# Optimization experiments

Measured on AMD Instinct MI355X. Metric: run time of the kernel, lower is better.

Reference implementation:

```python
import jax, jax.numpy as jnp
import numpy as np

GROUPS = 8
HEADS = 4
EPS = 1e-5


def setup_inputs() -> dict:
    key = jax.random.key(0)
    ks = jax.random.split(key, 3)
    b, c, h, w = 4, 256, 64, 64
    x = jax.random.normal(ks[0], (b, c, h, w), dtype=jnp.float32)
    gn_gamma = jnp.ones((c,), jnp.float32)
    gn_beta = jnp.zeros((c,), jnp.float32)
    w_qkv = jax.random.normal(ks[1], (3 * c, c), dtype=jnp.float32) * (c ** -0.5)
    w_proj = jax.random.normal(ks[2], (c, c), dtype=jnp.float32) * (c ** -0.5)
    b_proj = jnp.zeros((c,), jnp.float32)
    return {"x": x, "gn_gamma": gn_gamma, "gn_beta": gn_beta,
            "w_qkv": w_qkv, "w_proj": w_proj, "b_proj": b_proj}


def reference(x, gn_gamma, gn_beta, w_qkv, w_proj, b_proj):
    b, c, h, w = x.shape
    residual = x
    # GroupNorm(8, c)
    xg = x.reshape(b, GROUPS, -1)
    mean = jnp.mean(xg, axis=-1, keepdims=True)
    var = jnp.var(xg, axis=-1, keepdims=True)
    xn = ((xg - mean) * jax.lax.rsqrt(var + EPS)).reshape(b, c, h, w)
    xn = xn * gn_gamma[:, None, None] + gn_beta[:, None, None]
    # QKV conv1x1 (no bias)
    qkv = jnp.einsum('oc,bchw->bohw', w_qkv, xn)  # [b,3c,h,w]
    q, k, v = jnp.split(qkv, 3, axis=1)
    n = h * w
    dh = c // HEADS
    q = q.reshape(b, HEADS, dh, n)
    k = k.reshape(b, HEADS, dh, n)
    v = v.reshape(b, HEADS, dh, n)
    scale = (c * HEADS) ** (-0.5)
    attn = jnp.einsum('bhci,bhcj->bhij', q, k) * scale  # [b,H,n,n]
    attn = jax.nn.softmax(attn, axis=-1)
    out = jnp.einsum('bhij,bhcj->bhci', attn, v).reshape(b, c, h, w)
    out = jnp.einsum('oc,bchw->bohw', w_proj, out) + b_proj[:, None, None]
    return out + residual
```

## Files before the change

kernel.cpp:

```cpp
#include <hip/hip_runtime.h>
#include <math.h>
#include <stdint.h>

#define B_ 4
#define C_ 256
#define HW_ 4096
#define G_ 8
#define H_ 4
#define DH_ 64
#define GRP_ELEMS (32 * HW_)
#define NCHUNK 16
#define CHUNK_ELEMS (GRP_ELEMS / NCHUNK)
#define EPS 1e-5f
#define NT_ (HW_ / 64)
#define QSCALE 0.04508422f

typedef __attribute__((ext_vector_type(8))) short short8;
typedef __attribute__((ext_vector_type(4))) float f32x4;
typedef __attribute__((ext_vector_type(4))) unsigned int u32x4;
typedef const __attribute__((address_space(1))) uint32_t* gas1_t;
typedef __attribute__((address_space(3))) uint32_t* las3_t;

__device__ __forceinline__ ushort f2bf(float x) {
    unsigned u = __builtin_bit_cast(unsigned, x);
    u += 0x7FFFu + ((u >> 16) & 1u);
    return (ushort)(u >> 16);
}
__device__ __forceinline__ uint32_t cvt_pk_bf16(float lo, float hi) {
    uint32_t r;
    asm("v_cvt_pk_bf16_f32 %0, %1, %2" : "=v"(r) : "v"(lo), "v"(hi));
    return r;
}

__global__ __launch_bounds__(256) void gn_part_wcvt(const float* __restrict__ x,
                                                    float* __restrict__ part,
                                                    const float* __restrict__ wq,
                                                    const float* __restrict__ wp,
                                                    ushort* __restrict__ wqb,
                                                    ushort* __restrict__ wpb) {
    int t = threadIdx.x;
    if (blockIdx.x >= 512) {
        int i = (blockIdx.x - 512) * 256 + t;
        if (i < 768 * 256) {
            float s = (i < 256 * 256) ? QSCALE : 1.0f;
            wqb[i] = f2bf(wq[i] * s);
        } else {
            wpb[i - 768 * 256] = f2bf(wp[i - 768 * 256]);
        }
        return;
    }
    int bg = blockIdx.x >> 4;
    int chunk = blockIdx.x & 15;
    const float4* p = (const float4*)(x + (size_t)bg * GRP_ELEMS + (size_t)chunk * CHUNK_ELEMS);
    float s = 0.f, ss = 0.f;
#pragma unroll
    for (int i = 0; i < 8; ++i) {
        float4 v = p[t + i * 256];
        s  += v.x + v.y + v.z + v.w;
        ss += v.x * v.x + v.y * v.y + v.z * v.z + v.w * v.w;
    }
#pragma unroll
    for (int off = 32; off; off >>= 1) {
        s  += __shfl_xor(s, off, 64);
        ss += __shfl_xor(ss, off, 64);
    }
    __shared__ float ls[8];
    int wave = t >> 6, lane = t & 63;
    if (lane == 0) { ls[wave * 2] = s; ls[wave * 2 + 1] = ss; }
    __syncthreads();
    if (t == 0) {
        float S = 0.f, SS = 0.f;
#pragma unroll
        for (int w = 0; w < 4; ++w) { S += ls[w * 2]; SS += ls[w * 2 + 1]; }
        part[(bg * 16 + chunk) * 2]     = S;
        part[(bg * 16 + chunk) * 2 + 1] = SS;
    }
}

#define TSTR 264
__global__ __launch_bounds__(256) void gn_qkv(const float* __restrict__ x,
                                              const float* __restrict__ gamma,
                                              const float* __restrict__ beta,
                                              const float* __restrict__ part,
                                              const ushort* __restrict__ wqb,
                                              ushort* __restrict__ qt,
                                              ushort* __restrict__ kt,
                                              ushort* __restrict__ vv) {
    __shared__ float2 affs[256];
    __shared__ __align__(16) ushort Ts[64 * TSTR];
    int n0 = blockIdx.x * 64;
    int b  = blockIdx.y;
    int t = threadIdx.x;

    {
        int c = t;
        int bg = b * G_ + (c >> 5);
        float S = 0.f, SS = 0.f;
#pragma unroll
        for (int i = 0; i < 16; ++i) {
            S  += part[(bg * 16 + i) * 2];
            SS += part[(bg * 16 + i) * 2 + 1];
        }
        float mean = S * (1.f / GRP_ELEMS);
        float var  = SS * (1.f / GRP_ELEMS) - mean * mean;
        float inv  = rsqrtf(var + EPS);
        float a = inv * gamma[c];
        affs[c] = make_float2(a, beta[c] - mean * a);
    }
    __syncthreads();

    {
        int n4 = t & 15, cr = t >> 4;
#pragma unroll
        for (int ct = 0; ct < 16; ++ct) {
            int c = cr + 16 * ct;
            float2 p = affs[c];
            float4 v = *(const float4*)(x + ((size_t)(b * C_ + c)) * HW_ + n0 + n4 * 4);
            ushort e[4];
            e[0] = f2bf(v.x * p.x + p.y); e[1] = f2bf(v.y * p.x + p.y);
            e[2] = f2bf(v.z * p.x + p.y); e[3] = f2bf(v.w * p.x + p.y);
#pragma unroll
            for (int k = 0; k < 4; ++k) {
                int n = n4 * 4 + k;
                Ts[n * TSTR + (((c >> 3) ^ ((n >> 2) & 7)) << 3) + (c & 7)] = e[k];
            }
        }
    }
    __syncthreads();

    int w = t >> 6, lane = t & 63, l16 = lane & 15, lg = lane >> 4;

    for (int z = 0; z < 3; ++z) {
        const ushort* wz = wqb + (size_t)(z * 256 + 32 * w + l16) * C_;
        f32x4 acc[2][2][4];
#pragma unroll
        for (int j = 0; j < 2; ++j)
#pragma unroll
            for (int os = 0; os < 2; ++os)
#pragma unroll
                for (int u = 0; u < 4; ++u)
#pragma unroll
                    for (int r = 0; r < 4; ++r) acc[j][os][u][r] = 0.f;

#pragma unroll 2
        for (int ks = 0; ks < 8; ++ks) {
            short8 a00 = *(const short8*)(wz + 32 * ks + 8 * lg);
            short8 a01 = *(const short8*)(wz + 16 * C_ + 32 * ks + 8 * lg);
            short8 a10 = *(const short8*)(wz + 128 * C_ + 32 * ks + 8 * lg);
            short8 a11 = *(const short8*)(wz + 144 * C_ + 32 * ks + 8 * lg);
#pragma unroll
            for (int u = 0; u < 4; ++u) {
                int n = 16 * u + l16;
                short8 bf = *(const short8*)&Ts[n * TSTR +
                               (((4 * ks + lg) ^ ((n >> 2) & 7)) << 3)];
                acc[0][0][u] = __builtin_amdgcn_mfma_f32_16x16x32_bf16(a00, bf, acc[0][0][u], 0, 0, 0);
                acc[0][1][u] = __builtin_amdgcn_mfma_f32_16x16x32_bf16(a01, bf, acc[0][1][u], 0, 0, 0);
                acc[1][0][u] = __builtin_amdgcn_mfma_f32_16x16x32_bf16(a10, bf, acc[1][0][u], 0, 0, 0);
                acc[1][1][u] = __builtin_amdgcn_mfma_f32_16x16x32_bf16(a11, bf, acc[1][1][u], 0, 0, 0);
            }
        }

#pragma unroll
        for (int j = 0; j < 2; ++j)
#pragma unroll
            for (int os = 0; os < 2; ++os) {
                int o_base = z * 256 + 128 * j + 32 * w + 16 * os;
                if (z < 2) {
                    int h = (o_base >> 6) & 3;
                    int od0 = (o_base & 63) + 4 * lg;
                    ushort* dstb = (z ? kt : qt) + ((size_t)((b << 2) | h) * HW_) * DH_;
#pragma unroll
                    for (int u = 0; u < 4; ++u) {
                        int n = n0 + 16 * u + l16;
                        uint2 pk;
                        pk.x = cvt_pk_bf16(acc[j][os][u][0], acc[j][os][u][1]);
                        pk.y = cvt_pk_bf16(acc[j][os][u][2], acc[j][os][u][3]);
                        *(uint2*)(dstb + (size_t)n * DH_ + od0) = pk;
                    }
                } else {
                    int row0 = o_base - 512 + 4 * lg;
#pragma unroll
                    for (int u = 0; u < 4; ++u) {
                        int n = n0 + 16 * u + l16;
#pragma unroll
                        for (int r = 0; r < 4; ++r)
                            vv[((size_t)(b * C_ + row0 + r)) * HW_ + n] = f2bf(acc[j][os][u][r]);
                    }
                }
            }
    }
}

__global__ __launch_bounds__(256) void flash_attn_mfma(const ushort* __restrict__ qt,
                                                       const ushort* __restrict__ kt,
                                                       const ushort* __restrict__ vv,
                                                       ushort* __restrict__ attT) {
    __shared__ __align__(16) ushort Kb[3][64 * 64];
    __shared__ __align__(16) ushort Vb[3][64 * 64];

    int bid = blockIdx.x;
    int wg = (bid & 7) * 64 + (bid >> 3);
    int bh = wg >> 5;
    int i0 = (wg & 31) * 128;
    int b = bh >> 2, h = bh & 3;
    int t = threadIdx.x;
    int w = t >> 6, lane = t & 63, l16 = lane & 15, lg = lane >> 4;
    const ushort* qtb = qt + (size_t)bh * HW_ * DH_;
    const ushort* ktb = kt + (size_t)bh * HW_ * DH_;
    const ushort* vb  = vv + ((size_t)(b * C_) + h * DH_) * HW_;

    short8 qf[2][2];
#pragma unroll
    for (int s = 0; s < 2; ++s)
#pragma unroll
        for (int ks = 0; ks < 2; ++ks)
            qf[s][ks] = *(const short8*)(qtb + (size_t)(i0 + 32 * w + 16 * s + l16) * DH_ + 32 * ks + 8 * lg);

    f32x4 O0[4], O1[4], lacc0, lacc1;
#pragma unroll
    for (int dt = 0; dt < 4; ++dt)
#pragma unroll
        for (int r = 0; r < 4; ++r) { O0[dt][r] = 0.f; O1[dt][r] = 0.f; }
#pragma unroll
    for (int r = 0; r < 4; ++r) { lacc0[r] = 0.f; lacc1[r] = 0.f; }
    const f32x4 Z4 = {0.f, 0.f, 0.f, 0.f};

    u32x4 ov; ov[0] = ov[1] = ov[2] = ov[3] = 0x3F803F80u;
    short8 onesf = __builtin_bit_cast(short8, ov);

    int r8 = lane >> 3, ch8 = lane & 7;
    size_t koff[2], voff[2];
#pragma unroll
    for (int half = 0; half < 2; ++half) {
        int L = 16 * w + half * 8 + r8;
        int gk = (L & 0x23) | ((L & 0x0C) << 1) | ((L & 0x10) >> 2);
        koff[half] = (size_t)gk * DH_ + ((ch8 ^ (L & 7)) << 3);
        voff[half] = (size_t)L * HW_ + ((ch8 ^ (L & 7)) << 3);
    }

    auto stageK = [&](int bi, int j0) {
#pragma unroll
        for (int half = 0; half < 2; ++half) {
            int rowb = 16 * w + half * 8;
            __builtin_amdgcn_global_load_lds((gas1_t)(ktb + (size_t)j0 * DH_ + koff[half]),
                (las3_t)&Kb[bi][rowb * 64], 16, 0, 0);
        }
    };
    auto stageV = [&](int bi, int j0) {
#pragma unroll
        for (int half = 0; half < 2; ++half) {
            int rowb = 16 * w + half * 8;
            __builtin_amdgcn_global_load_lds((gas1_t)(vb + (size_t)j0 + voff[half]),
                (las3_t)&Vb[bi][rowb * 64], 16, 0, 0);
        }
    };

    auto qk2 = [&](int bi, f32x4* S0, f32x4* S1) {
        __builtin_amdgcn_s_setprio(1);
#pragma unroll
        for (int jt = 0; jt < 4; ++jt) {
            short8 kf0 = *(const short8*)&Kb[bi][(16 * jt + l16) * 64 +
                                                ((lg ^ (l16 & 7)) << 3)];
            S0[jt] = __builtin_amdgcn_mfma_f32_16x16x32_bf16(kf0, qf[0][0], Z4, 0, 0, 0);
            S1[jt] = __builtin_amdgcn_mfma_f32_16x16x32_bf16(kf0, qf[1][0], Z4, 0, 0, 0);
            short8 kf1 = *(const short8*)&Kb[bi][(16 * jt + l16) * 64 +
                                                (((4 + lg) ^ (l16 & 7)) << 3)];
            S0[jt] = __builtin_amdgcn_mfma_f32_16x16x32_bf16(kf1, qf[0][1], S0[jt], 0, 0, 0);
            S1[jt] = __builtin_amdgcn_mfma_f32_16x16x32_bf16(kf1, qf[1][1], S1[jt], 0, 0, 0);
        }
        __builtin_amdgcn_s_setprio(0);
    };

    auto pv2 = [&](int bi, short8* pf0, short8* pf1) {
        __builtin_amdgcn_s_setprio(1);
#pragma unroll
        for (int dt = 0; dt < 4; ++dt) {
#pragma unroll
            for (int ks = 0; ks < 2; ++ks) {
                short8 vf = *(const short8*)&Vb[bi][(16 * dt + l16) * 64 +
                                                    (((4 * ks + lg) ^ (l16 & 7)) << 3)];
                O0[dt] = __builtin_amdgcn_mfma_f32_16x16x32_bf16(vf, pf0[ks], O0[dt], 0, 0, 0);
                O1[dt] = __builtin_amdgcn_mfma_f32_16x16x32_bf16(vf, pf1[ks], O1[dt], 0, 0, 0);
            }
        }
        lacc0 = __builtin_amdgcn_mfma_f32_16x16x32_bf16(onesf, pf0[0], lacc0, 0, 0, 0);
        lacc0 = __builtin_amdgcn_mfma_f32_16x16x32_bf16(onesf, pf0[1], lacc0, 0, 0, 0);
        lacc1 = __builtin_amdgcn_mfma_f32_16x16x32_bf16(onesf, pf1[0], lacc1, 0, 0, 0);
        lacc1 = __builtin_amdgcn_mfma_f32_16x16x32_bf16(onesf, pf1[1], lacc1, 0, 0, 0);
        __builtin_amdgcn_s_setprio(0);
    };

    auto softmax_pf = [&](f32x4* S, short8* pf) {
#pragma unroll
        for (int jt = 0; jt < 4; ++jt)
#pragma unroll
            for (int r = 0; r < 4; ++r)
                S[jt][r] = __builtin_amdgcn_exp2f(S[jt][r]);
#pragma unroll
        for (int ks = 0; ks < 2; ++ks) {
            u32x4 p;
            p[0] = cvt_pk_bf16(S[2 * ks][0],     S[2 * ks][1]);
            p[1] = cvt_pk_bf16(S[2 * ks][2],     S[2 * ks][3]);
            p[2] = cvt_pk_bf16(S[2 * ks + 1][0], S[2 * ks + 1][1]);
            p[3] = cvt_pk_bf16(S[2 * ks + 1][2], S[2 * ks + 1][3]);
            pf[ks] = __builtin_bit_cast(short8, p);
        }
    };

    f32x4 Sa0[4], Sa1[4], Sb0[4], Sb1[4];

    auto body = [&](int VW, int KR, int KW, int VR,
                    f32x4* SC0, f32x4* SC1, f32x4* SN0, f32x4* SN1,
                    int tt, int drain) {
        if (tt + 2 < NT_) stageV(VW, (tt + 2) * 64);
        qk2(KR, SN0, SN1);
        if (tt + 3 < NT_) stageK(KW, (tt + 3) * 64);
        short8 pf0[2], pf1[2];
        softmax_pf(SC0, pf0);
        softmax_pf(SC1, pf1);
        pv2(VR, pf0, pf1);
        if (drain == 4) asm volatile("s_waitcnt vmcnt(4)" ::: "memory");
        else            asm volatile("s_waitcnt vmcnt(0)" ::: "memory");
        __builtin_amdgcn_s_barrier();
    };

    stageK(0, 0); stageV(0, 0);
    stageK(1, 64); stageV(1, 64);
    stageK(2, 128);
    asm volatile("s_waitcnt vmcnt(0)" ::: "memory");
    __builtin_amdgcn_s_barrier();
    qk2(0, Sa0, Sa1);
    __builtin_amdgcn_s_barrier();

    for (int g = 0; g < 10; ++g) {
        int tb = 6 * g;
        body(2, 1, 0, 0, Sa0, Sa1, Sb0, Sb1, tb + 0, 4);
        body(0, 2, 1, 1, Sb0, Sb1, Sa0, Sa1, tb + 1, 4);
        body(1, 0, 2, 2, Sa0, Sa1, Sb0, Sb1, tb + 2, 4);
        body(2, 1, 0, 0, Sb0, Sb1, Sa0, Sa1, tb + 3, 4);
        body(0, 2, 1, 1, Sa0, Sa1, Sb0, Sb1, tb + 4, 4);
        body(1, 0, 2, 2, Sb0, Sb1, Sa0, Sa1, tb + 5, 4);
    }
    body(2, 1, 0, 0, Sa0, Sa1, Sb0, Sb1, 60, 4);
    body(0, 2, 1, 1, Sb0, Sb1, Sa0, Sa1, 61, 4);
    body(1, 0, 2, 2, Sa0, Sa1, Sb0, Sb1, 62, 0);
    {
        short8 pf0[2], pf1[2];
        softmax_pf(Sb0, pf0);
        softmax_pf(Sb1, pf1);
        pv2(0, pf0, pf1);
    }

    float inv0 = 1.f / lacc0[0], inv1 = 1.f / lacc1[0];
    ushort* ab0 = attT + ((size_t)b * HW_ + i0 + 32 * w + l16) * C_ + h * DH_;
    ushort* ab1 = ab0 + 16 * C_;
#pragma unroll
    for (int dt = 0; dt < 4; ++dt) {
        uint2 p0, p1;
        p0.x = cvt_pk_bf16(O0[dt][0] * inv0, O0[dt][1] * inv0);
        p0.y = cvt_pk_bf16(O0[dt][2] * inv0, O0[dt][3] * inv0);
        *(uint2*)(ab0 + 16 * dt + 4 * lg) = p0;
        p1.x = cvt_pk_bf16(O1[dt][0] * inv1, O1[dt][1] * inv1);
        p1.y = cvt_pk_bf16(O1[dt][2] * inv1, O1[dt][3] * inv1);
        *(uint2*)(ab1 + 16 * dt + 4 * lg) = p1;
    }
}

__global__ __launch_bounds__(256) void proj_gemm(const ushort* __restrict__ wpb,
                                                 const ushort* __restrict__ attT,
                                                 const float* __restrict__ bias,
                                                 const float* __restrict__ x,
                                                 float* __restrict__ out) {
    __shared__ __align__(16) ushort Ts[64 * TSTR];
    int n0 = blockIdx.x * 64;
    int o0 = blockIdx.y * 128;
    int b  = blockIdx.z;
    int t = threadIdx.x;
    int w = t >> 6, lane = t & 63, l16 = lane & 15, lg = lane >> 4;
    const ushort* xb = attT + ((size_t)b * HW_ + n0) * C_;

    {
#pragma unroll
        for (int i = 0; i < 8; ++i) {
            int q = t + 256 * i;
            int n = q >> 5, c8 = q & 31;
            uint4 v = *(const uint4*)(xb + (size_t)n * C_ + c8 * 8);
            *(uint4*)&Ts[n * TSTR + ((c8 ^ ((n >> 2) & 7)) << 3)] = v;
        }
    }
    __syncthreads();

    const ushort* wrow0 = wpb + (size_t)(o0 + 32 * w + l16) * C_;
    const ushort* wrow1 = wrow0 + 16 * C_;

    f32x4 acc[2][4];
#pragma unroll
    for (int os = 0; os < 2; ++os)
#pragma unroll
        for (int u = 0; u < 4; ++u)
#pragma unroll
            for (int r = 0; r < 4; ++r) acc[os][u][r] = 0.f;

#pragma unroll 2
    for (int ks = 0; ks < 8; ++ks) {
        short8 a0 = *(const short8*)(wrow0 + 32 * ks + 8 * lg);
        short8 a1 = *(const short8*)(wrow1 + 32 * ks + 8 * lg);
#pragma unroll
        for (int u = 0; u < 4; ++u) {
            int n = 16 * u + l16;
            short8 bf = *(const short8*)&Ts[n * TSTR +
                           (((4 * ks + lg) ^ ((n >> 2) & 7)) << 3)];
            acc[0][u] = __builtin_amdgcn_mfma_f32_16x16x32_bf16(a0, bf, acc[0][u], 0, 0, 0);
            acc[1][u] = __builtin_amdgcn_mfma_f32_16x16x32_bf16(a1, bf, acc[1][u], 0, 0, 0);
        }
    }

#pragma unroll
    for (int os = 0; os < 2; ++os) {
        int o_base = o0 + 32 * w + 16 * os;
#pragma unroll
        for (int u = 0; u < 4; ++u) {
            int n = n0 + 16 * u + l16;
#pragma unroll
            for (int r = 0; r < 4; ++r) {
                int mrow = o_base + 4 * lg + r;
                size_t idx = ((size_t)(b * C_ + mrow)) * HW_ + n;
                out[idx] = acc[os][u][r] + bias[mrow] + x[idx];
            }
        }
    }
}

extern "C" void kernel_launch(void* const* d_in, const int* in_sizes, int n_in,
                              void* d_out, int out_size, void* d_ws, size_t ws_size,
                              hipStream_t stream) {
    const float* x        = (const float*)d_in[0];
    const float* gn_gamma = (const float*)d_in[1];
    const float* gn_beta  = (const float*)d_in[2];
    const float* w_qkv    = (const float*)d_in[3];
    const float* w_proj   = (const float*)d_in[4];
    const float* b_proj   = (const float*)d_in[5];
    float* out = (float*)d_out;

    ushort* wsp  = (ushort*)d_ws;
    ushort* qt   = wsp;
    ushort* kt   = qt   + 4194304;
    ushort* vv   = kt   + 4194304;
    ushort* attT = vv   + 4194304;
    ushort* wqb  = attT + 4194304;
    ushort* wpb  = wqb  + 196608;
    float*  part = (float*)(wpb + 65536);

    gn_part_wcvt<<<dim3(512 + 1024), 256, 0, stream>>>(x, part, w_qkv, w_proj, wqb, wpb);
    gn_qkv<<<dim3(HW_ / 64, B_), 256, 0, stream>>>(x, gn_gamma, gn_beta, part, wqb, qt, kt, vv);
    flash_attn_mfma<<<dim3(512), 256, 0, stream>>>(qt, kt, vv, attT);
    proj_gemm<<<dim3(HW_ / 64, 2, B_), 256, 0, stream>>>(wpb, attT, b_proj, x, out);
}
```

Measured before the change: 116.5 us.

## Split attention KV range in two halves with separate combine kernel

Each attention block now processes half of the key/value sequence, doubling the grid to 1024 blocks and writing unnormalized fp32 partial outputs and row sums. A new combine kernel sums the two partials, normalizes, and converts to bf16 for the projection GEMM. This aims to raise occupancy and parallelism per CU, at the cost of extra fp32 global traffic and an additional kernel launch.

```diff
diff --git a/kernel.cpp b/kernel.cpp
--- a/kernel.cpp
+++ b/kernel.cpp
@@ -12,7 +12,7 @@
 #define NCHUNK 16
 #define CHUNK_ELEMS (GRP_ELEMS / NCHUNK)
 #define EPS 1e-5f
-#define NT_ (HW_ / 64)
+#define NTH_ 32
 #define QSCALE 0.04508422f
 
 typedef __attribute__((ext_vector_type(8))) short short8;
@@ -194,14 +194,18 @@
 __global__ __launch_bounds__(256) void flash_attn_mfma(const ushort* __restrict__ qt,
                                                        const ushort* __restrict__ kt,
                                                        const ushort* __restrict__ vv,
-                                                       ushort* __restrict__ attT) {
+                                                       float* __restrict__ Opart,
+                                                       float* __restrict__ lpart) {
     __shared__ __align__(16) ushort Kb[3][64 * 64];
     __shared__ __align__(16) ushort Vb[3][64 * 64];
 
     int bid = blockIdx.x;
-    int wg = (bid & 7) * 64 + (bid >> 3);
-    int bh = wg >> 5;
-    int i0 = (wg & 31) * 128;
+    int wg = (bid & 7) * 128 + (bid >> 3);
+    int bh = wg >> 6;
+    int it = (wg >> 1) & 31;
+    int jh = wg & 1;
+    int i0 = it * 128;
+    int jbase = jh * (NTH_ * 64);
     int b = bh >> 2, h = bh & 3;
     int t = threadIdx.x;
     int w = t >> 6, lane = t & 63, l16 = lane & 15, lg = lane >> 4;
@@ -312,27 +316,28 @@
     auto body = [&](int VW, int KR, int KW, int VR,
                     f32x4* SC0, f32x4* SC1, f32x4* SN0, f32x4* SN1,
                     int tt, int drain) {
-        if (tt + 2 < NT_) stageV(VW, (tt + 2) * 64);
+        if (tt + 2 < NTH_) stageV(VW, jbase + (tt + 2) * 64);
         qk2(KR, SN0, SN1);
-        if (tt + 3 < NT_) stageK(KW, (tt + 3) * 64);
+        if (tt + 3 < NTH_) stageK(KW, jbase + (tt + 3) * 64);
         short8 pf0[2], pf1[2];
         softmax_pf(SC0, pf0);
         softmax_pf(SC1, pf1);
         pv2(VR, pf0, pf1);
-        if (drain == 4) asm volatile("s_waitcnt vmcnt(4)" ::: "memory");
-        else            asm volatile("s_waitcnt vmcnt(0)" ::: "memory");
+        if (drain == 4)      asm volatile("s_waitcnt vmcnt(4)" ::: "memory");
+        else if (drain == 2) asm volatile("s_waitcnt vmcnt(2)" ::: "memory");
+        else                 asm volatile("s_waitcnt vmcnt(0)" ::: "memory");
         __builtin_amdgcn_s_barrier();
     };
 
-    stageK(0, 0); stageV(0, 0);
-    stageK(1, 64); stageV(1, 64);
-    stageK(2, 128);
+    stageK(0, jbase); stageV(0, jbase);
+    stageK(1, jbase + 64); stageV(1, jbase + 64);
+    stageK(2, jbase + 128);
     asm volatile("s_waitcnt vmcnt(0)" ::: "memory");
     __builtin_amdgcn_s_barrier();
     qk2(0, Sa0, Sa1);
     __builtin_amdgcn_s_barrier();
 
-    for (int g = 0; g < 10; ++g) {
+    for (int g = 0; g < 4; ++g) {
         int tb = 6 * g;
         body(2, 1, 0, 0, Sa0, Sa1, Sb0, Sb1, tb + 0, 4);
         body(0, 2, 1, 1, Sb0, Sb1, Sa0, Sa1, tb + 1, 4);
@@ -341,29 +346,62 @@
         body(0, 2, 1, 1, Sa0, Sa1, Sb0, Sb1, tb + 4, 4);
         body(1, 0, 2, 2, Sb0, Sb1, Sa0, Sa1, tb + 5, 4);
     }
-    body(2, 1, 0, 0, Sa0, Sa1, Sb0, Sb1, 60, 4);
-    body(0, 2, 1, 1, Sb0, Sb1, Sa0, Sa1, 61, 4);
-    body(1, 0, 2, 2, Sa0, Sa1, Sb0, Sb1, 62, 0);
+    body(2, 1, 0, 0, Sa0, Sa1, Sb0, Sb1, 24, 4);
+    body(0, 2, 1, 1, Sb0, Sb1, Sa0, Sa1, 25, 4);
+    body(1, 0, 2, 2, Sa0, Sa1, Sb0, Sb1, 26, 4);
+    body(2, 1, 0, 0, Sb0, Sb1, Sa0, Sa1, 27, 4);
+    body(0, 2, 1, 1, Sa0, Sa1, Sb0, Sb1, 28, 4);
+    body(1, 0, 2, 2, Sb0, Sb1, Sa0, Sa1, 29, 2);
+    body(2, 1, 0, 0, Sa0, Sa1, Sb0, Sb1, 30, 0);
     {
         short8 pf0[2], pf1[2];
         softmax_pf(Sb0, pf0);
         softmax_pf(Sb1, pf1);
-        pv2(0, pf0, pf1);
-    }
-
-    float inv0 = 1.f / lacc0[0], inv1 = 1.f / lacc1[0];
-    ushort* ab0 = attT + ((size_t)b * HW_ + i0 + 32 * w + l16) * C_ + h * DH_;
-    ushort* ab1 = ab0 + 16 * C_;
+        pv2(1, pf0, pf1);
+    }
+
+    float* o0p = Opart + (size_t)jh * (size_t)(B_ * C_ * HW_) +
+                 ((size_t)(b * HW_) + i0 + 32 * w + l16) * C_ + h * DH_;
+    float* o1p = o0p + 16 * C_;
 #pragma unroll
     for (int dt = 0; dt < 4; ++dt) {
-        uint2 p0, p1;
-        p0.x = cvt_pk_bf16(O0[dt][0] * inv0, O0[dt][1] * inv0);
-        p0.y = cvt_pk_bf16(O0[dt][2] * inv0, O0[dt][3] * inv0);
-        *(uint2*)(ab0 + 16 * dt + 4 * lg) = p0;
-        p1.x = cvt_pk_bf16(O1[dt][0] * inv1, O1[dt][1] * inv1);
-        p1.y = cvt_pk_bf16(O1[dt][2] * inv1, O1[dt][3] * inv1);
-        *(uint2*)(ab1 + 16 * dt + 4 * lg) = p1;
-    }
+        *(f32x4*)(o0p + 16 * dt + 4 * lg) = O0[dt];
+        *(f32x4*)(o1p + 16 * dt + 4 * lg) = O1[dt];
+    }
+    if (lg == 0) {
+        float* lp = lpart + (size_t)jh * (size_t)(4 * B_ * HW_) + (size_t)bh * HW_;
+        lp[i0 + 32 * w + l16]      = lacc0[0];
+        lp[i0 + 32 * w + 16 + l16] = lacc1[0];
+    }
+}
+
+__global__ __launch_bounds__(256) void combine(const float* __restrict__ Opart,
+                                               const float* __restrict__ lpart,
+                                               ushort* __restrict__ attT) {
+    int e = blockIdx.x * 256 + threadIdx.x;
+    size_t base = (size_t)e * 8;
+    int row = e >> 5;
+    int c0 = (e & 31) * 8;
+    int h = c0 >> 6;
+    int bb = row >> 12, i = row & 4095;
+    size_t lidx = ((size_t)(bb * 4 + h)) * HW_ + i;
+    const float* l0 = lpart;
+    const float* l1 = lpart + (size_t)(4 * B_ * HW_);
+    float inv = 1.f / (l0[lidx] + l1[lidx]);
+    const float* O0 = Opart;
+    const float* O1 = Opart + (size_t)(B_ * C_ * HW_);
+    f32x4 a = *(const f32x4*)(O0 + base);
+    f32x4 b2 = *(const f32x4*)(O1 + base);
+    f32x4 c = *(const f32x4*)(O0 + base + 4);
+    f32x4 d = *(const f32x4*)(O1 + base + 4);
+#pragma unroll
+    for (int r = 0; r < 4; ++r) { a[r] = (a[r] + b2[r]) * inv; c[r] = (c[r] + d[r]) * inv; }
+    u32x4 o;
+    o[0] = cvt_pk_bf16(a[0], a[1]);
+    o[1] = cvt_pk_bf16(a[2], a[3]);
+    o[2] = cvt_pk_bf16(c[0], c[1]);
+    o[3] = cvt_pk_bf16(c[2], c[3]);
+    *(u32x4*)(attT + base) = o;
 }
 
 __global__ __launch_bounds__(256) void proj_gemm(const ushort* __restrict__ wpb,
@@ -450,9 +488,12 @@
     ushort* wqb  = attT + 4194304;
     ushort* wpb  = wqb  + 196608;
     float*  part = (float*)(wpb + 65536);
+    float*  Opart = part + 512;
+    float*  lpart = Opart + 2 * 4194304;
 
     gn_part_wcvt<<<dim3(512 + 1024), 256, 0, stream>>>(x, part, w_qkv, w_proj, wqb, wpb);
     gn_qkv<<<dim3(HW_ / 64, B_), 256, 0, stream>>>(x, gn_gamma, gn_beta, part, wqb, qt, kt, vv);
-    flash_attn_mfma<<<dim3(512), 256, 0, stream>>>(qt, kt, vv, attT);
+    flash_attn_mfma<<<dim3(1024), 256, 0, stream>>>(qt, kt, vv, Opart, lpart);
+    combine<<<dim3(2048), 256, 0, stream>>>(Opart, lpart, attT);
     proj_gemm<<<dim3(HW_ / 64, 2, B_), 256, 0, stream>>>(wpb, attT, b_proj, x, out);
 }
```

Measured after the change: 121.6 us. 4.3% more time.
